# Kernel tuning notes

Measured on AMD Instinct MI355X. Metric: run time of the kernel, lower is better.

## Reference

```python
import jax, jax.numpy as jnp
import numpy as np


def _forward(f2e_emb, score_mat, rel_features, Wk, bk,
             batch_heads, batch_rels, batch_tails, edge_mat, eps):
    B, N, D = f2e_emb.shape
    R = rel_features.shape[0]
    dt = f2e_emb.dtype
    # -cdist(x, x) then row softmax (F.softmax dim=1 on a 2D mat == last axis)
    x2 = jnp.sum(f2e_emb * f2e_emb, axis=-1)                              # [B,N]
    d2 = x2[:, :, None] + x2[:, None, :] - 2.0 * jnp.einsum('bnd,bmd->bnm', f2e_emb, f2e_emb)
    sim = jax.nn.softmax(-jnp.sqrt(jnp.maximum(d2, 0.0)), axis=-1)        # [B,N,N]
    prob = jnp.einsum('bnk,bmk->bnm', sim, score_mat)                     # sim @ score_mat.T
    cand = (prob > eps) & (edge_mat < 1)                                  # candidate (row,col) pairs
    # torch.multinomial(sim[row], 1) per candidate pair -> gumbel-max categorical,
    # one independent draw per (b, row, col) over the row's similarity distribution
    logits = jnp.log(sim)[:, :, None, :]                                  # [B,N,1,N]
    s = jax.random.categorical(jax.random.key(42),
                               jax.lax.stop_gradient(jnp.broadcast_to(logits, (B, N, N, N))),
                               axis=-1)                                    # [B,N,N]
    b3 = jnp.arange(B)[:, None, None]
    r3 = jnp.arange(N)[None, :, None]
    c3 = jnp.arange(N)[None, None, :]
    new_rel = edge_mat[b3, s, c3]                                          # [B,N,N]
    valid = (cand & (new_rel != 0)).astype(dt)
    # per-(node, relation) incidence counts: exactly equivalent to the
    # fact2head_mat/fact2tail_mat sparse.mm aggregation of kb_self_linear(rel_features[rel])
    counts = jnp.zeros((B * N * R,), dt)
    counts = counts.at[((b3 * N + r3) * R + new_rel).ravel()].add(valid.ravel())  # new edge -> head
    counts = counts.at[((b3 * N + c3) * R + new_rel).ravel()].add(valid.ravel())  # new edge -> tail
    b2 = jnp.arange(B)[:, None]
    ones = jnp.ones(batch_heads.shape, dt)
    counts = counts.at[((b2 * N + batch_heads) * R + batch_rels).ravel()].add(ones.ravel())
    counts = counts.at[((b2 * N + batch_tails) * R + batch_rels).ravel()].add(ones.ravel())
    counts = counts.reshape(B, N, R)
    Wr = rel_features @ Wk + bk                                            # kb_self_linear(rel_features) [R,O]
    return jax.nn.relu(jnp.einsum('bnr,ro->bno', counts, Wr))              # [B,N,O]


def setup_inputs():
    key = jax.random.key(0)
    ks = jax.random.split(key, 10)
    B, N, D, O, R, E = 8, 256, 256, 256, 512, 8192
    return {
        'f2e_emb': jax.random.normal(ks[0], (B, N, D), jnp.float32),
        'score_mat': jax.random.normal(ks[1], (B, N, N), jnp.float32),
        'rel_features': jax.random.normal(ks[2], (R, D), jnp.float32),
        'Wk': jax.random.normal(ks[3], (D, O), jnp.float32) / np.sqrt(D).astype(np.float32),
        'bk': jnp.zeros((O,), jnp.float32),
        'local_entity': jax.random.randint(ks[4], (B, N), 0, N, jnp.int32),
        'batch_heads': jax.random.randint(ks[5], (B, E), 0, N, jnp.int32),
        'batch_rels': jax.random.randint(ks[6], (B, E), 0, R, jnp.int32),
        'batch_tails': jax.random.randint(ks[7], (B, E), 0, N, jnp.int32),
        'edge_mat': jax.random.randint(ks[8], (B, N, N), 0, 4, jnp.int32),
        'eps': 0,
    }


def reference(f2e_emb, score_mat, rel_features, Wk, bk, local_entity,
              batch_heads, batch_rels, batch_tails, edge_mat, eps):
    return _forward(f2e_emb, score_mat, rel_features, Wk, bk,
                    batch_heads, batch_rels, batch_tails, edge_mat, eps)
```

## Files before the change

kernel.cpp:

```cpp
#include <hip/hip_runtime.h>
#include <stdint.h>

#define B 8
#define N 256
#define D 256
#define O 256
#define R 512
#define E 8192
#define NSW 8192
#define F32_TINY 1.17549435e-38f

__device__ __forceinline__ void threefry2x32_k42(uint32_t x0, uint32_t x1,
                                                 uint32_t& o0, uint32_t& o1) {
  const uint32_t ks0 = 0u;
  const uint32_t ks1 = 42u;
  const uint32_t ks2 = 0u ^ 42u ^ 0x1BD11BDAu;
  x0 += ks0; x1 += ks1;
#define TF_R(r) { x0 += x1; x1 = (x1 << (r)) | (x1 >> (32 - (r))); x1 ^= x0; }
  TF_R(13) TF_R(15) TF_R(26) TF_R(6)
  x0 += ks1; x1 += ks2 + 1u;
  TF_R(17) TF_R(29) TF_R(16) TF_R(24)
  x0 += ks2; x1 += ks0 + 2u;
  TF_R(13) TF_R(15) TF_R(26) TF_R(6)
  x0 += ks0; x1 += ks1 + 3u;
  TF_R(17) TF_R(29) TF_R(16) TF_R(24)
  x0 += ks1; x1 += ks2 + 4u;
  TF_R(13) TF_R(15) TF_R(26) TF_R(6)
  x0 += ks2; x1 += ks0 + 5u;
#undef TF_R
  o0 = x0; o1 = x1;
}

__device__ __forceinline__ float gumbel_from_bits_f(float f) {
  float u = (f == 0.0f) ? F32_TINY : f;
  return -logf(-logf(u));
}

#define LOADT(PANEL, KK)                                                      \
  { const float* gp_ = (PANEL) + (size_t)((KK) * 16 + srow) * 256 + scol;     \
    st0 = *(const float4*)gp_; gp_ += 1024;                                   \
    st1 = *(const float4*)gp_; gp_ += 1024;                                   \
    st2 = *(const float4*)gp_; gp_ += 1024;                                   \
    st3 = *(const float4*)gp_; }
#define WRITET()                                                              \
  { *(float4*)&buf[srow][scol]      = st0;                                    \
    *(float4*)&buf[srow + 4][scol]  = st1;                                    \
    *(float4*)&buf[srow + 8][scol]  = st2;                                    \
    *(float4*)&buf[srow + 12][scol] = st3; }

__global__ __launch_bounds__(256) void prep_kernel(const float* __restrict__ score,
                                                   float* __restrict__ scoreT,
                                                   const float* __restrict__ f2e,
                                                   float* __restrict__ f2eT,
                                                   const float* __restrict__ relf,
                                                   const float* __restrict__ Wk,
                                                   const float* __restrict__ bk,
                                                   float* __restrict__ Wr,
                                                   float* __restrict__ x2,
                                                   int* __restrict__ wcount) {
  int blk = blockIdx.x;
  int tid = threadIdx.x;
  if (blk == 0 && tid == 0) *wcount = 0;
  if (blk < 256) {
    __shared__ float tile[64][65];
    const float* src = (blk < 128) ? score : f2e;
    float* dst = (blk < 128) ? scoreT : f2eT;
    int b7 = blk & 127;
    int bb = b7 & 7, t = b7 >> 3, ti = t >> 2, tj = t & 3;
    size_t base = (size_t)bb * 65536;
    int c = tid & 63, r4 = tid >> 6;
#pragma unroll
    for (int rr = 0; rr < 64; rr += 4) {
      int row = rr + r4;
      tile[row][c] = src[base + (size_t)(ti * 64 + row) * 256 + tj * 64 + c];
    }
    __syncthreads();
#pragma unroll
    for (int rr = 0; rr < 64; rr += 4) {
      int row = rr + r4;
      dst[base + (size_t)(tj * 64 + row) * 256 + ti * 64 + c] = tile[c][row];
    }
  } else if (blk < 512) {
    __shared__ float rrow[2][D];
    __shared__ float buf[16][256];
    int r0 = (blk - 256) * 2;
    int srow = tid >> 6, scol = (tid & 63) * 4;
    float4 st0, st1, st2, st3;
    rrow[0][tid] = relf[(size_t)r0 * D + tid];
    rrow[1][tid] = relf[(size_t)(r0 + 1) * D + tid];
    float aA0 = 0.f, aB0 = 0.f, aA1 = 0.f, aB1 = 0.f;
    LOADT(Wk, 0);
    for (int kk = 0; kk < 16; ++kk) {
      __syncthreads();
      WRITET();
      __syncthreads();
      if (kk < 15) LOADT(Wk, kk + 1);
      int dbase = kk * 16;
#pragma unroll
      for (int dd = 0; dd < 16; dd += 4) {
        float4 a0 = *(const float4*)&rrow[0][dbase + dd];
        float4 a1 = *(const float4*)&rrow[1][dbase + dd];
        float b0 = buf[dd + 0][tid], b1 = buf[dd + 1][tid];
        float b2 = buf[dd + 2][tid], b3 = buf[dd + 3][tid];
        aA0 += a0.x * b0; aB0 += a0.y * b1; aA0 += a0.z * b2; aB0 += a0.w * b3;
        aA1 += a1.x * b0; aB1 += a1.y * b1; aA1 += a1.z * b2; aB1 += a1.w * b3;
      }
    }
    float bv = bk[tid];
    Wr[(size_t)r0 * O + tid] = (aA0 + aB0) + bv;
    Wr[(size_t)(r0 + 1) * O + tid] = (aA1 + aB1) + bv;
  } else {
    int i = (blk - 512) * 256 + tid;
    const float4* p = (const float4*)(f2e + (size_t)i * D);
    double s = 0.0;
    for (int d = 0; d < D / 4; ++d) {
      float4 v = p[d];
      s += (double)v.x * v.x; s += (double)v.y * v.y;
      s += (double)v.z * v.z; s += (double)v.w * v.w;
    }
    x2[i] = (float)s;
  }
}

__global__ __launch_bounds__(256) void simcand_kernel(const float* __restrict__ f2e,
                                                      const float* __restrict__ f2eT,
                                                      const float* __restrict__ x2,
                                                      const float* __restrict__ scoreT,
                                                      const int* __restrict__ edge,
                                                      const int* __restrict__ epsp,
                                                      float* __restrict__ logits,
                                                      float* __restrict__ laux,
                                                      int* __restrict__ wlist,
                                                      int* __restrict__ wcount) {
  int bid = blockIdx.x;
  int b = bid & 7;
  int bn0 = b * 256 + (bid >> 3) * 2;
  int tid = threadIdx.x, lane = tid & 63, w = tid >> 6;
  __shared__ float arow[2][256];
  __shared__ float simrow[2][256];
  __shared__ float buf[16][256];
  __shared__ float wred[2][4];
  __shared__ double dred[2][4];
  __shared__ float lnsh[2];
  int srow = tid >> 6, scol = (tid & 63) * 4;
  float4 st0, st1, st2, st3;
  arow[0][tid] = f2e[(size_t)bn0 * 256 + tid];
  arow[1][tid] = f2e[(size_t)(bn0 + 1) * 256 + tid];
  const float* panelF = f2eT + (size_t)b * 65536;
  float aA0 = 0.f, aB0 = 0.f, aA1 = 0.f, aB1 = 0.f;
  LOADT(panelF, 0);
  for (int kk = 0; kk < 16; ++kk) {
    __syncthreads();
    WRITET();
    __syncthreads();
    if (kk < 15) LOADT(panelF, kk + 1);
    int dbase = kk * 16;
#pragma unroll
    for (int dd = 0; dd < 16; dd += 4) {
      float4 a0 = *(const float4*)&arow[0][dbase + dd];
      float4 a1 = *(const float4*)&arow[1][dbase + dd];
      float b0 = buf[dd + 0][tid], b1 = buf[dd + 1][tid];
      float b2 = buf[dd + 2][tid], b3 = buf[dd + 3][tid];
      aA0 += a0.x * b0; aB0 += a0.y * b1; aA0 += a0.z * b2; aB0 += a0.w * b3;
      aA1 += a1.x * b0; aB1 += a1.y * b1; aA1 += a1.z * b2; aB1 += a1.w * b3;
    }
  }
  const float* panelS = scoreT + (size_t)b * 65536;
  LOADT(panelS, 0);
  float x2c = x2[b * 256 + tid];
  float neg0 = -sqrtf(fmaxf((x2[bn0] + x2c) - 2.0f * (aA0 + aB0), 0.0f));
  float neg1 = -sqrtf(fmaxf((x2[bn0 + 1] + x2c) - 2.0f * (aA1 + aB1), 0.0f));
  float m0 = neg0, m1 = neg1;
#pragma unroll
  for (int off = 32; off > 0; off >>= 1) {
    m0 = fmaxf(m0, __shfl_xor(m0, off));
    m1 = fmaxf(m1, __shfl_xor(m1, off));
  }
  if (lane == 0) { wred[0][w] = m0; wred[1][w] = m1; }
  __syncthreads();
  float mx0 = fmaxf(fmaxf(wred[0][0], wred[0][1]), fmaxf(wred[0][2], wred[0][3]));
  float mx1 = fmaxf(fmaxf(wred[1][0], wred[1][1]), fmaxf(wred[1][2], wred[1][3]));
  float p0 = expf(neg0 - mx0), p1 = expf(neg1 - mx1);
  double s0 = (double)p0, s1 = (double)p1;
#pragma unroll
  for (int off = 32; off > 0; off >>= 1) {
    s0 += __shfl_xor(s0, off);
    s1 += __shfl_xor(s1, off);
  }
  if (lane == 0) { dred[0][w] = s0; dred[1][w] = s1; }
  __syncthreads();
  float den0 = (float)(dred[0][0] + dred[0][1] + dred[0][2] + dred[0][3]);
  float den1 = (float)(dred[1][0] + dred[1][1] + dred[1][2] + dred[1][3]);
  float sv0 = p0 / den0, sv1 = p1 / den1;
  simrow[0][tid] = sv0; simrow[1][tid] = sv1;
  float l0 = logf(sv0), l1 = logf(sv1);
  logits[(size_t)bn0 * 256 + tid] = l0;
  logits[(size_t)(bn0 + 1) * 256 + tid] = l1;
  int d0 = bn0 & 255, d1 = (bn0 + 1) & 255;
  if (tid == d0) lnsh[0] = l0;
  if (tid == d1) lnsh[1] = l1;
  float e0 = (tid == d0) ? -3.4e38f : l0;
  float e1 = (tid == d1) ? -3.4e38f : l1;
#pragma unroll
  for (int off = 32; off > 0; off >>= 1) {
    e0 = fmaxf(e0, __shfl_xor(e0, off));
    e1 = fmaxf(e1, __shfl_xor(e1, off));
  }
  if (lane == 0) { wred[0][w] = e0; wred[1][w] = e1; }
  __syncthreads();
  if (tid == 0) {
    laux[2 * bn0 + 0] = lnsh[0];
    laux[2 * bn0 + 1] = fmaxf(fmaxf(wred[0][0], wred[0][1]), fmaxf(wred[0][2], wred[0][3]));
    laux[2 * bn0 + 2] = lnsh[1];
    laux[2 * bn0 + 3] = fmaxf(fmaxf(wred[1][0], wred[1][1]), fmaxf(wred[1][2], wred[1][3]));
  }
  float pA0 = 0.f, pB0 = 0.f, pA1 = 0.f, pB1 = 0.f;
  for (int kk = 0; kk < 16; ++kk) {
    __syncthreads();
    WRITET();
    __syncthreads();
    if (kk < 15) LOADT(panelS, kk + 1);
    int kbase = kk * 16;
#pragma unroll
    for (int dd = 0; dd < 16; dd += 4) {
      float4 q0 = *(const float4*)&simrow[0][kbase + dd];
      float4 q1 = *(const float4*)&simrow[1][kbase + dd];
      float b0 = buf[dd + 0][tid], b1 = buf[dd + 1][tid];
      float b2 = buf[dd + 2][tid], b3 = buf[dd + 3][tid];
      pA0 += q0.x * b0; pB0 += q0.y * b1; pA0 += q0.z * b2; pB0 += q0.w * b3;
      pA1 += q1.x * b0; pB1 += q1.y * b1; pA1 += q1.z * b2; pB1 += q1.w * b3;
    }
  }
  float epsv = (float)epsp[0];
  float pr[2] = {pA0 + pB0, pA1 + pB1};
#pragma unroll
  for (int r = 0; r < 2; ++r) {
    int row = (bn0 + r) * 256 + tid;
    int em = edge[(size_t)row];
    bool active = (pr[r] > epsv) && (em < 1);
    unsigned long long mask = __ballot(active);
    int cnt = __popcll(mask);
    int basev = 0;
    if (lane == 0 && cnt) basev = atomicAdd(wcount, cnt);
    basev = __shfl(basev, 0);
    if (active) {
      int pos = basev + __popcll(mask & ((1ull << lane) - 1ull));
      wlist[pos] = row;
    }
  }
}

__global__ __launch_bounds__(256) void sample_kernel(const float* __restrict__ logits,
                                                     const float* __restrict__ laux,
                                                     const int* __restrict__ wlist,
                                                     const int* __restrict__ wcount,
                                                     const int* __restrict__ edge,
                                                     const int* __restrict__ heads,
                                                     const int* __restrict__ rels,
                                                     const int* __restrict__ tails,
                                                     float* __restrict__ counts) {
  int blk = blockIdx.x;
  if (blk >= 2048) {
    int i = (blk - 2048) * 256 + threadIdx.x;
    int b = i >> 13;
    int h = heads[i], r = rels[i], t = tails[i];
    atomicAdd(&counts[(size_t)(b * N + h) * R + r], 1.0f);
    atomicAdd(&counts[(size_t)(b * N + t) * R + r], 1.0f);
    return;
  }
  int lane = threadIdx.x & 63;
  int gw = blk * 4 + (threadIdx.x >> 6);
  int cnt = *wcount;
  for (int idx = gw; idx < cnt; idx += NSW) {
    int row = wlist[idx];
    int b = row >> 16;
    int n = (row >> 8) & 255;
    int c = row & 255;
    uint32_t base = (uint32_t)row << 8;
    float u0, u1, u2, u3;
    {
      uint32_t a0, a1;
#define GEN_U(q, dst)                                                     \
      threefry2x32_k42(0u, base + (uint32_t)((q) * 64 + lane), a0, a1);    \
      dst = __uint_as_float((((a0 ^ a1) >> 9)) | 0x3f800000u) - 1.0f;
      GEN_U(0, u0) GEN_U(1, u1) GEN_U(2, u2) GEN_U(3, u3)
#undef GEN_U
    }
    float l_n  = laux[2 * ((b << 8) + n) + 0];
    float Lmax = laux[2 * ((b << 8) + n) + 1];
    int qo = n >> 6;
    float uo = (qo == 0) ? u0 : (qo == 1) ? u1 : (qo == 2) ? u2 : u3;
    float u_n = __shfl(uo, n & 63);
    float v_n = gumbel_from_bits_f(u_n) + l_n;
    float thr_g = (v_n - Lmax) - 0.125f;
    float u_thr = expf(-expf(-thr_g));
    bool owner = (lane == (n & 63));
    bool anyc = ((u0 > u_thr) && !(owner && qo == 0)) |
                ((u1 > u_thr) && !(owner && qo == 1)) |
                ((u2 > u_thr) && !(owner && qo == 2)) |
                ((u3 > u_thr) && !(owner && qo == 3));
    if (!__any(anyc)) continue;

    const float* lrow = logits + (size_t)((b << 8) + n) * N;
    float bestv = -1e30f;
    int besti = 0;
    for (int q = 0; q < 4; ++q) {
      int k = q * 64 + lane;
      uint32_t o0, o1;
      threefry2x32_k42(0u, base + (uint32_t)k, o0, o1);
      uint32_t bits = o0 ^ o1;
      float f = __uint_as_float((bits >> 9) | 0x3f800000u) - 1.0f;
      float g = gumbel_from_bits_f(f);
      float v = g + lrow[k];
      if (v > bestv || (v == bestv && k < besti)) { bestv = v; besti = k; }
    }
    for (int off = 32; off > 0; off >>= 1) {
      float ov = __shfl_down(bestv, off);
      int oi = __shfl_down(besti, off);
      if (ov > bestv || (ov == bestv && oi < besti)) { bestv = ov; besti = oi; }
    }
    if (lane == 0) {
      int nr = edge[(size_t)((b << 8) + besti) * N + c];
      if (nr != 0) {
        atomicAdd(&counts[(size_t)((b << 8) + n) * R + nr], 1.0f);
        atomicAdd(&counts[(size_t)((b << 8) + c) * R + nr], 1.0f);
      }
    }
  }
}

__global__ __launch_bounds__(256) void out_kernel(const float* __restrict__ counts,
                                                  const float* __restrict__ Wr,
                                                  float* __restrict__ out) {
  int bn0 = blockIdx.x * 4;
  int tid = threadIdx.x;
  __shared__ float crow[4][512];
  __shared__ float buf[16][256];
  int srow = tid >> 6, scol = (tid & 63) * 4;
  float4 st0, st1, st2, st3;
  {
    const float4* src = (const float4*)(counts + (size_t)bn0 * 512);
    float* flat = &crow[0][0];
    *(float4*)&flat[tid * 4] = src[tid];
    *(float4*)&flat[1024 + tid * 4] = src[256 + tid];
  }
  float accA[4] = {0, 0, 0, 0}, accB[4] = {0, 0, 0, 0};
  LOADT(Wr, 0);
  for (int kk = 0; kk < 32; ++kk) {
    __syncthreads();
    WRITET();
    __syncthreads();
    if (kk < 31) LOADT(Wr, kk + 1);
    int kbase = kk * 16;
#pragma unroll
    for (int dd = 0; dd < 16; dd += 4) {
      float b0 = buf[dd + 0][tid], b1 = buf[dd + 1][tid];
      float b2 = buf[dd + 2][tid], b3 = buf[dd + 3][tid];
#pragma unroll
      for (int r = 0; r < 4; ++r) {
        float4 cv = *(const float4*)&crow[r][kbase + dd];
        accA[r] += cv.x * b0; accB[r] += cv.y * b1;
        accA[r] += cv.z * b2; accB[r] += cv.w * b3;
      }
    }
  }
#pragma unroll
  for (int r = 0; r < 4; ++r)
    out[(size_t)(bn0 + r) * O + tid] = fmaxf(accA[r] + accB[r], 0.0f);
}

extern "C" void kernel_launch(void* const* d_in, const int* in_sizes, int n_in,
                              void* d_out, int out_size, void* d_ws, size_t ws_size,
                              hipStream_t stream) {
  (void)in_sizes; (void)n_in; (void)out_size; (void)ws_size;
  const float* f2e   = (const float*)d_in[0];
  const float* score = (const float*)d_in[1];
  const float* relf  = (const float*)d_in[2];
  const float* Wk    = (const float*)d_in[3];
  const float* bk    = (const float*)d_in[4];
  const int* heads   = (const int*)d_in[6];
  const int* rels    = (const int*)d_in[7];
  const int* tails   = (const int*)d_in[8];
  const int* edge    = (const int*)d_in[9];
  const int* epsp    = (const int*)d_in[10];
  float* out = (float*)d_out;

  float* ws     = (float*)d_ws;
  float* logits = ws;
  float* Wr     = logits + 524288;
  float* counts = Wr + 131072;
  float* scoreT = counts;
  float* f2eT   = counts + 524288;
  float* laux   = counts + 1048576;
  float* x2     = laux + 4096;
  int*   wlist  = (int*)(x2 + 2048);
  int*   wcount = wlist + 524288;

  prep_kernel<<<520, 256, 0, stream>>>(score, scoreT, f2e, f2eT,
                                       relf, Wk, bk, Wr, x2, wcount);
  simcand_kernel<<<(B * N) / 2, 256, 0, stream>>>(f2e, f2eT, x2, scoreT, edge, epsp,
                                                  logits, laux, wlist, wcount);
  hipMemsetAsync(counts, 0, (size_t)B * N * R * sizeof(float), stream);
  sample_kernel<<<2048 + 256, 256, 0, stream>>>(logits, laux, wlist, wcount, edge,
                                                heads, rels, tails, counts);
  out_kernel<<<(B * N) / 4, 256, 0, stream>>>(counts, Wr, out);
}
```

Baseline: 205.3 us.

## Use 16-row 4x4 register-blocked tiles in the three matmul kernels

Replaces the 2- and 4-row per-block matmuls (Wr, similarity/prob, output) with 16-row blocks where each thread computes a 4x4 outer-product tile. This cuts the number of times each B panel is reloaded into shared memory and raises arithmetic per LDS load. The softmax reductions are rewritten to work per 4-row group with warp shuffles only. The cost is far fewer blocks (128 for simcand, 128 for out), which leaves most of the GPU's CUs idle, and more shared memory per block.

```diff
diff --git a/kernel.cpp b/kernel.cpp
--- a/kernel.cpp
+++ b/kernel.cpp
@@ -48,6 +48,30 @@
     *(float4*)&buf[srow + 8][scol]  = st2;                                    \
     *(float4*)&buf[srow + 12][scol] = st3; }
 
+#define OUTER4(AX, BV)                                                        \
+  acc[0][0] += a0.AX * BV.x; acc[0][1] += a0.AX * BV.y;                       \
+  acc[0][2] += a0.AX * BV.z; acc[0][3] += a0.AX * BV.w;                       \
+  acc[1][0] += a1.AX * BV.x; acc[1][1] += a1.AX * BV.y;                       \
+  acc[1][2] += a1.AX * BV.z; acc[1][3] += a1.AX * BV.w;                       \
+  acc[2][0] += a2.AX * BV.x; acc[2][1] += a2.AX * BV.y;                       \
+  acc[2][2] += a2.AX * BV.z; acc[2][3] += a2.AX * BV.w;                       \
+  acc[3][0] += a3.AX * BV.x; acc[3][1] += a3.AX * BV.y;                       \
+  acc[3][2] += a3.AX * BV.z; acc[3][3] += a3.AX * BV.w;
+
+#define TILE_COMPUTE(ASRC, KK)                                                \
+  _Pragma("unroll")                                                           \
+  for (int k4 = 0; k4 < 16; k4 += 4) {                                        \
+    float4 a0 = *(const float4*)&ASRC[r0 + 0][(KK) * 16 + k4];                \
+    float4 a1 = *(const float4*)&ASRC[r0 + 1][(KK) * 16 + k4];                \
+    float4 a2 = *(const float4*)&ASRC[r0 + 2][(KK) * 16 + k4];                \
+    float4 a3 = *(const float4*)&ASRC[r0 + 3][(KK) * 16 + k4];                \
+    float4 b0 = *(const float4*)&buf[k4 + 0][c0];                             \
+    float4 b1 = *(const float4*)&buf[k4 + 1][c0];                             \
+    float4 b2 = *(const float4*)&buf[k4 + 2][c0];                             \
+    float4 b3 = *(const float4*)&buf[k4 + 3][c0];                             \
+    OUTER4(x, b0) OUTER4(y, b1) OUTER4(z, b2) OUTER4(w, b3)                   \
+  }
+
 __global__ __launch_bounds__(256) void prep_kernel(const float* __restrict__ score,
                                                    float* __restrict__ scoreT,
                                                    const float* __restrict__ f2e,
@@ -60,6 +84,7 @@
                                                    int* __restrict__ wcount) {
   int blk = blockIdx.x;
   int tid = threadIdx.x;
+  __shared__ float buf[16][256];
   if (blk == 0 && tid == 0) *wcount = 0;
   if (blk < 256) {
     __shared__ float tile[64][65];
@@ -80,37 +105,39 @@
       int row = rr + r4;
       dst[base + (size_t)(tj * 64 + row) * 256 + ti * 64 + c] = tile[c][row];
     }
-  } else if (blk < 512) {
-    __shared__ float rrow[2][D];
-    __shared__ float buf[16][256];
-    int r0 = (blk - 256) * 2;
+  } else if (blk < 288) {
+    __shared__ float arel[16][256];
+    int rb0 = (blk - 256) * 16;
+    int g = tid >> 6, lane = tid & 63;
+    int r0 = 4 * g, c0 = 4 * lane;
     int srow = tid >> 6, scol = (tid & 63) * 4;
     float4 st0, st1, st2, st3;
-    rrow[0][tid] = relf[(size_t)r0 * D + tid];
-    rrow[1][tid] = relf[(size_t)(r0 + 1) * D + tid];
-    float aA0 = 0.f, aB0 = 0.f, aA1 = 0.f, aB1 = 0.f;
+#pragma unroll
+    for (int r = 0; r < 16; ++r)
+      arel[r][tid] = relf[(size_t)(rb0 + r) * 256 + tid];
+    float acc[4][4];
+#pragma unroll
+    for (int i = 0; i < 4; ++i)
+#pragma unroll
+      for (int j = 0; j < 4; ++j) acc[i][j] = 0.f;
     LOADT(Wk, 0);
     for (int kk = 0; kk < 16; ++kk) {
       __syncthreads();
       WRITET();
       __syncthreads();
       if (kk < 15) LOADT(Wk, kk + 1);
-      int dbase = kk * 16;
-#pragma unroll
-      for (int dd = 0; dd < 16; dd += 4) {
-        float4 a0 = *(const float4*)&rrow[0][dbase + dd];
-        float4 a1 = *(const float4*)&rrow[1][dbase + dd];
-        float b0 = buf[dd + 0][tid], b1 = buf[dd + 1][tid];
-        float b2 = buf[dd + 2][tid], b3 = buf[dd + 3][tid];
-        aA0 += a0.x * b0; aB0 += a0.y * b1; aA0 += a0.z * b2; aB0 += a0.w * b3;
-        aA1 += a1.x * b0; aB1 += a1.y * b1; aA1 += a1.z * b2; aB1 += a1.w * b3;
-      }
-    }
-    float bv = bk[tid];
-    Wr[(size_t)r0 * O + tid] = (aA0 + aB0) + bv;
-    Wr[(size_t)(r0 + 1) * O + tid] = (aA1 + aB1) + bv;
+      TILE_COMPUTE(arel, kk)
+    }
+    float4 bk4 = *(const float4*)&bk[c0];
+#pragma unroll
+    for (int rj = 0; rj < 4; ++rj) {
+      float4 o;
+      o.x = acc[rj][0] + bk4.x; o.y = acc[rj][1] + bk4.y;
+      o.z = acc[rj][2] + bk4.z; o.w = acc[rj][3] + bk4.w;
+      *(float4*)&Wr[(size_t)(rb0 + r0 + rj) * 256 + c0] = o;
+    }
   } else {
-    int i = (blk - 512) * 256 + tid;
+    int i = (blk - 288) * 256 + tid;
     const float4* p = (const float4*)(f2e + (size_t)i * D);
     double s = 0.0;
     for (int d = 0; d < D / 4; ++d) {
@@ -134,118 +161,109 @@
                                                       int* __restrict__ wcount) {
   int bid = blockIdx.x;
   int b = bid & 7;
-  int bn0 = b * 256 + (bid >> 3) * 2;
-  int tid = threadIdx.x, lane = tid & 63, w = tid >> 6;
-  __shared__ float arow[2][256];
-  __shared__ float simrow[2][256];
+  int bn0 = b * 256 + (bid >> 3) * 16;
+  int tid = threadIdx.x;
+  int g = tid >> 6, lane = tid & 63;
+  int r0 = 4 * g, c0 = 4 * lane;
+  __shared__ float arow[16][256];
+  __shared__ float simrow[16][256];
   __shared__ float buf[16][256];
-  __shared__ float wred[2][4];
-  __shared__ double dred[2][4];
-  __shared__ float lnsh[2];
   int srow = tid >> 6, scol = (tid & 63) * 4;
   float4 st0, st1, st2, st3;
-  arow[0][tid] = f2e[(size_t)bn0 * 256 + tid];
-  arow[1][tid] = f2e[(size_t)(bn0 + 1) * 256 + tid];
+#pragma unroll
+  for (int r = 0; r < 16; ++r)
+    arow[r][tid] = f2e[(size_t)(bn0 + r) * 256 + tid];
   const float* panelF = f2eT + (size_t)b * 65536;
-  float aA0 = 0.f, aB0 = 0.f, aA1 = 0.f, aB1 = 0.f;
+  float acc[4][4];
+#pragma unroll
+  for (int i = 0; i < 4; ++i)
+#pragma unroll
+    for (int j = 0; j < 4; ++j) acc[i][j] = 0.f;
   LOADT(panelF, 0);
   for (int kk = 0; kk < 16; ++kk) {
     __syncthreads();
     WRITET();
     __syncthreads();
     if (kk < 15) LOADT(panelF, kk + 1);
-    int dbase = kk * 16;
-#pragma unroll
-    for (int dd = 0; dd < 16; dd += 4) {
-      float4 a0 = *(const float4*)&arow[0][dbase + dd];
-      float4 a1 = *(const float4*)&arow[1][dbase + dd];
-      float b0 = buf[dd + 0][tid], b1 = buf[dd + 1][tid];
-      float b2 = buf[dd + 2][tid], b3 = buf[dd + 3][tid];
-      aA0 += a0.x * b0; aB0 += a0.y * b1; aA0 += a0.z * b2; aB0 += a0.w * b3;
-      aA1 += a1.x * b0; aB1 += a1.y * b1; aA1 += a1.z * b2; aB1 += a1.w * b3;
-    }
+    TILE_COMPUTE(arow, kk)
   }
   const float* panelS = scoreT + (size_t)b * 65536;
   LOADT(panelS, 0);
-  float x2c = x2[b * 256 + tid];
-  float neg0 = -sqrtf(fmaxf((x2[bn0] + x2c) - 2.0f * (aA0 + aB0), 0.0f));
-  float neg1 = -sqrtf(fmaxf((x2[bn0 + 1] + x2c) - 2.0f * (aA1 + aB1), 0.0f));
-  float m0 = neg0, m1 = neg1;
-#pragma unroll
-  for (int off = 32; off > 0; off >>= 1) {
-    m0 = fmaxf(m0, __shfl_xor(m0, off));
-    m1 = fmaxf(m1, __shfl_xor(m1, off));
-  }
-  if (lane == 0) { wred[0][w] = m0; wred[1][w] = m1; }
-  __syncthreads();
-  float mx0 = fmaxf(fmaxf(wred[0][0], wred[0][1]), fmaxf(wred[0][2], wred[0][3]));
-  float mx1 = fmaxf(fmaxf(wred[1][0], wred[1][1]), fmaxf(wred[1][2], wred[1][3]));
-  float p0 = expf(neg0 - mx0), p1 = expf(neg1 - mx1);
-  double s0 = (double)p0, s1 = (double)p1;
-#pragma unroll
-  for (int off = 32; off > 0; off >>= 1) {
-    s0 += __shfl_xor(s0, off);
-    s1 += __shfl_xor(s1, off);
-  }
-  if (lane == 0) { dred[0][w] = s0; dred[1][w] = s1; }
-  __syncthreads();
-  float den0 = (float)(dred[0][0] + dred[0][1] + dred[0][2] + dred[0][3]);
-  float den1 = (float)(dred[1][0] + dred[1][1] + dred[1][2] + dred[1][3]);
-  float sv0 = p0 / den0, sv1 = p1 / den1;
-  simrow[0][tid] = sv0; simrow[1][tid] = sv1;
-  float l0 = logf(sv0), l1 = logf(sv1);
-  logits[(size_t)bn0 * 256 + tid] = l0;
-  logits[(size_t)(bn0 + 1) * 256 + tid] = l1;
-  int d0 = bn0 & 255, d1 = (bn0 + 1) & 255;
-  if (tid == d0) lnsh[0] = l0;
-  if (tid == d1) lnsh[1] = l1;
-  float e0 = (tid == d0) ? -3.4e38f : l0;
-  float e1 = (tid == d1) ? -3.4e38f : l1;
-#pragma unroll
-  for (int off = 32; off > 0; off >>= 1) {
-    e0 = fmaxf(e0, __shfl_xor(e0, off));
-    e1 = fmaxf(e1, __shfl_xor(e1, off));
-  }
-  if (lane == 0) { wred[0][w] = e0; wred[1][w] = e1; }
-  __syncthreads();
-  if (tid == 0) {
-    laux[2 * bn0 + 0] = lnsh[0];
-    laux[2 * bn0 + 1] = fmaxf(fmaxf(wred[0][0], wred[0][1]), fmaxf(wred[0][2], wred[0][3]));
-    laux[2 * bn0 + 2] = lnsh[1];
-    laux[2 * bn0 + 3] = fmaxf(fmaxf(wred[1][0], wred[1][1]), fmaxf(wred[1][2], wred[1][3]));
-  }
-  float pA0 = 0.f, pB0 = 0.f, pA1 = 0.f, pB1 = 0.f;
+  float4 x2c4 = *(const float4*)&x2[b * 256 + c0];
+  float sv[4][4], lg[4][4];
+#pragma unroll
+  for (int rj = 0; rj < 4; ++rj) {
+    float x2r = x2[bn0 + r0 + rj];
+    float n0 = -sqrtf(fmaxf((x2r + x2c4.x) - 2.0f * acc[rj][0], 0.0f));
+    float n1 = -sqrtf(fmaxf((x2r + x2c4.y) - 2.0f * acc[rj][1], 0.0f));
+    float n2 = -sqrtf(fmaxf((x2r + x2c4.z) - 2.0f * acc[rj][2], 0.0f));
+    float n3 = -sqrtf(fmaxf((x2r + x2c4.w) - 2.0f * acc[rj][3], 0.0f));
+    float m = fmaxf(fmaxf(n0, n1), fmaxf(n2, n3));
+#pragma unroll
+    for (int off = 32; off > 0; off >>= 1) m = fmaxf(m, __shfl_xor(m, off));
+    float p0 = expf(n0 - m), p1 = expf(n1 - m), p2 = expf(n2 - m), p3 = expf(n3 - m);
+    double s = (((double)p0 + (double)p1) + (double)p2) + (double)p3;
+#pragma unroll
+    for (int off = 32; off > 0; off >>= 1) s += __shfl_xor(s, off);
+    float den = (float)s;
+    sv[rj][0] = p0 / den; sv[rj][1] = p1 / den;
+    sv[rj][2] = p2 / den; sv[rj][3] = p3 / den;
+    lg[rj][0] = logf(sv[rj][0]); lg[rj][1] = logf(sv[rj][1]);
+    lg[rj][2] = logf(sv[rj][2]); lg[rj][3] = logf(sv[rj][3]);
+  }
+#pragma unroll
+  for (int rj = 0; rj < 4; ++rj) {
+    int row_g = bn0 + r0 + rj;
+    float4 s4; s4.x = sv[rj][0]; s4.y = sv[rj][1]; s4.z = sv[rj][2]; s4.w = sv[rj][3];
+    *(float4*)&simrow[r0 + rj][c0] = s4;
+    float4 l4; l4.x = lg[rj][0]; l4.y = lg[rj][1]; l4.z = lg[rj][2]; l4.w = lg[rj][3];
+    *(float4*)&logits[(size_t)row_g * 256 + c0] = l4;
+    int diagc = row_g & 255;
+    int cjd = diagc & 3, laned = diagc >> 2;
+    float lsel = (cjd == 0) ? lg[rj][0] : (cjd == 1) ? lg[rj][1]
+               : (cjd == 2) ? lg[rj][2] : lg[rj][3];
+    float l_n = __shfl(lsel, laned);
+    float e0 = (c0 + 0 == diagc) ? -3.4e38f : lg[rj][0];
+    float e1 = (c0 + 1 == diagc) ? -3.4e38f : lg[rj][1];
+    float e2 = (c0 + 2 == diagc) ? -3.4e38f : lg[rj][2];
+    float e3 = (c0 + 3 == diagc) ? -3.4e38f : lg[rj][3];
+    float Lm = fmaxf(fmaxf(e0, e1), fmaxf(e2, e3));
+#pragma unroll
+    for (int off = 32; off > 0; off >>= 1) Lm = fmaxf(Lm, __shfl_xor(Lm, off));
+    if (lane == 0) {
+      laux[2 * row_g + 0] = l_n;
+      laux[2 * row_g + 1] = Lm;
+    }
+  }
+#pragma unroll
+  for (int i = 0; i < 4; ++i)
+#pragma unroll
+    for (int j = 0; j < 4; ++j) acc[i][j] = 0.f;
   for (int kk = 0; kk < 16; ++kk) {
     __syncthreads();
     WRITET();
     __syncthreads();
     if (kk < 15) LOADT(panelS, kk + 1);
-    int kbase = kk * 16;
-#pragma unroll
-    for (int dd = 0; dd < 16; dd += 4) {
-      float4 q0 = *(const float4*)&simrow[0][kbase + dd];
-      float4 q1 = *(const float4*)&simrow[1][kbase + dd];
-      float b0 = buf[dd + 0][tid], b1 = buf[dd + 1][tid];
-      float b2 = buf[dd + 2][tid], b3 = buf[dd + 3][tid];
-      pA0 += q0.x * b0; pB0 += q0.y * b1; pA0 += q0.z * b2; pB0 += q0.w * b3;
-      pA1 += q1.x * b0; pB1 += q1.y * b1; pA1 += q1.z * b2; pB1 += q1.w * b3;
-    }
+    TILE_COMPUTE(simrow, kk)
   }
   float epsv = (float)epsp[0];
-  float pr[2] = {pA0 + pB0, pA1 + pB1};
-#pragma unroll
-  for (int r = 0; r < 2; ++r) {
-    int row = (bn0 + r) * 256 + tid;
-    int em = edge[(size_t)row];
-    bool active = (pr[r] > epsv) && (em < 1);
-    unsigned long long mask = __ballot(active);
-    int cnt = __popcll(mask);
-    int basev = 0;
-    if (lane == 0 && cnt) basev = atomicAdd(wcount, cnt);
-    basev = __shfl(basev, 0);
-    if (active) {
-      int pos = basev + __popcll(mask & ((1ull << lane) - 1ull));
-      wlist[pos] = row;
+#pragma unroll
+  for (int rj = 0; rj < 4; ++rj) {
+    int row_g = bn0 + r0 + rj;
+    int4 ev = *(const int4*)&edge[(size_t)row_g * 256 + c0];
+#pragma unroll
+    for (int cj = 0; cj < 4; ++cj) {
+      int e = (cj == 0) ? ev.x : (cj == 1) ? ev.y : (cj == 2) ? ev.z : ev.w;
+      bool active = (acc[rj][cj] > epsv) && (e < 1);
+      unsigned long long mask = __ballot(active);
+      int cnt = __popcll(mask);
+      int basev = 0;
+      if (lane == 0 && cnt) basev = atomicAdd(wcount, cnt);
+      basev = __shfl(basev, 0);
+      if (active) {
+        int pos = basev + __popcll(mask & ((1ull << lane) - 1ull));
+        wlist[pos] = row_g * 256 + (c0 + cj);
+      }
     }
   }
 }
@@ -332,41 +350,39 @@
 __global__ __launch_bounds__(256) void out_kernel(const float* __restrict__ counts,
                                                   const float* __restrict__ Wr,
                                                   float* __restrict__ out) {
-  int bn0 = blockIdx.x * 4;
+  int bn0 = blockIdx.x * 16;
   int tid = threadIdx.x;
-  __shared__ float crow[4][512];
+  int g = tid >> 6, lane = tid & 63;
+  int r0 = 4 * g, c0 = 4 * lane;
+  __shared__ float crow[16][512];
   __shared__ float buf[16][256];
   int srow = tid >> 6, scol = (tid & 63) * 4;
   float4 st0, st1, st2, st3;
-  {
-    const float4* src = (const float4*)(counts + (size_t)bn0 * 512);
-    float* flat = &crow[0][0];
-    *(float4*)&flat[tid * 4] = src[tid];
-    *(float4*)&flat[1024 + tid * 4] = src[256 + tid];
-  }
-  float accA[4] = {0, 0, 0, 0}, accB[4] = {0, 0, 0, 0};
+#pragma unroll
+  for (int r = 0; r < 16; ++r) {
+    crow[r][tid] = counts[(size_t)(bn0 + r) * 512 + tid];
+    crow[r][256 + tid] = counts[(size_t)(bn0 + r) * 512 + 256 + tid];
+  }
+  float acc[4][4];
+#pragma unroll
+  for (int i = 0; i < 4; ++i)
+#pragma unroll
+    for (int j = 0; j < 4; ++j) acc[i][j] = 0.f;
   LOADT(Wr, 0);
   for (int kk = 0; kk < 32; ++kk) {
     __syncthreads();
     WRITET();
     __syncthreads();
     if (kk < 31) LOADT(Wr, kk + 1);
-    int kbase = kk * 16;
-#pragma unroll
-    for (int dd = 0; dd < 16; dd += 4) {
-      float b0 = buf[dd + 0][tid], b1 = buf[dd + 1][tid];
-      float b2 = buf[dd + 2][tid], b3 = buf[dd + 3][tid];
-#pragma unroll
-      for (int r = 0; r < 4; ++r) {
-        float4 cv = *(const float4*)&crow[r][kbase + dd];
-        accA[r] += cv.x * b0; accB[r] += cv.y * b1;
-        accA[r] += cv.z * b2; accB[r] += cv.w * b3;
-      }
-    }
-  }
-#pragma unroll
-  for (int r = 0; r < 4; ++r)
-    out[(size_t)(bn0 + r) * O + tid] = fmaxf(accA[r] + accB[r], 0.0f);
+    TILE_COMPUTE(crow, kk)
+  }
+#pragma unroll
+  for (int rj = 0; rj < 4; ++rj) {
+    float4 o;
+    o.x = fmaxf(acc[rj][0], 0.0f); o.y = fmaxf(acc[rj][1], 0.0f);
+    o.z = fmaxf(acc[rj][2], 0.0f); o.w = fmaxf(acc[rj][3], 0.0f);
+    *(float4*)&out[(size_t)(bn0 + r0 + rj) * 256 + c0] = o;
+  }
 }
 
 extern "C" void kernel_launch(void* const* d_in, const int* in_sizes, int n_in,
@@ -396,12 +412,12 @@
   int*   wlist  = (int*)(x2 + 2048);
   int*   wcount = wlist + 524288;
 
-  prep_kernel<<<520, 256, 0, stream>>>(score, scoreT, f2e, f2eT,
+  prep_kernel<<<296, 256, 0, stream>>>(score, scoreT, f2e, f2eT,
                                        relf, Wk, bk, Wr, x2, wcount);
-  simcand_kernel<<<(B * N) / 2, 256, 0, stream>>>(f2e, f2eT, x2, scoreT, edge, epsp,
-                                                  logits, laux, wlist, wcount);
+  simcand_kernel<<<128, 256, 0, stream>>>(f2e, f2eT, x2, scoreT, edge, epsp,
+                                          logits, laux, wlist, wcount);
   hipMemsetAsync(counts, 0, (size_t)B * N * R * sizeof(float), stream);
   sample_kernel<<<2048 + 256, 256, 0, stream>>>(logits, laux, wlist, wcount, edge,
                                                 heads, rels, tails, counts);
-  out_kernel<<<(B * N) / 4, 256, 0, stream>>>(counts, Wr, out);
-}
+  out_kernel<<<(B * N) / 16, 256, 0, stream>>>(counts, Wr, out);
+}
```

Result: slower. 212.6 us (+3.5%).
